# Optimization experiments

Measured on AMD Instinct MI355X. Metric: run time of the kernel, lower is better.

Reference implementation:

```python
import jax, jax.numpy as jnp
import numpy as np

DIM = 512
HEADS = 8
DIM_HEAD = 64
DIM_INNER = HEADS * DIM_HEAD
SCALE = DIM_HEAD ** -0.5


def setup_inputs() -> dict:
    key = jax.random.key(0)
    ks = jax.random.split(key, 8)
    b, n = 2, 1024
    x = jax.random.normal(ks[0], (b, n, DIM), dtype=jnp.float32)
    w = lambda k, i, o: jax.random.normal(k, (i, o), dtype=jnp.float32) * 0.02
    return {
        'x': x,
        'w_q_u': w(ks[1], DIM, DIM_INNER),
        'w_k_u': w(ks[2], DIM, DIM_INNER),
        'w_v_u': w(ks[3], DIM, DIM_INNER),
        'w_q_c': w(ks[4], DIM, DIM_INNER),
        'w_k_c': w(ks[5], DIM, DIM_INNER),
        'w_v_c': w(ks[6], DIM, DIM_INNER),
        'w_out': w(ks[7], DIM_INNER, DIM),
    }


def reference(x, w_q_u, w_k_u, w_v_u, w_q_c, w_k_c, w_v_c, w_out):
    b, n, _ = x.shape

    def proj(w):  # [b,n,dim] -> [b,h,n,d]
        return (x @ w).reshape(b, n, HEADS, DIM_HEAD).transpose(0, 2, 1, 3)

    q_u, k_u, v_u = proj(w_q_u), proj(w_k_u), proj(w_v_u)
    q_c, k_c, v_c = proj(w_q_c), proj(w_k_c), proj(w_v_c)

    idx = jnp.arange(n)
    causal = idx[:, None] >= idx[None, :]  # tril ones (binary causal mask)

    # term1 = (q_c @ v_u^T) * scale, zeroed above diagonal
    term1 = jnp.einsum('bhid,bhjd->bhij', q_c, v_u) * SCALE
    term1 = term1 * causal.astype(term1.dtype)

    # sigmoid term: (q_u @ k_u^T)*scale with lookahead mask tril(-inf, diag=0)
    logits_u = jnp.einsum('bhid,bhjd->bhij', q_u, k_u) * SCALE
    sig = jax.nn.sigmoid(jnp.where(causal, -jnp.inf, logits_u))

    # S_u[i,k] = sum_j term1[i,j] * sig[k,j]
    S_u = jnp.einsum('bhij,bhkj->bhik', term1, sig)

    # S_c: causal-masked QK
    S_c = jnp.einsum('bhid,bhjd->bhij', q_c, k_c) * SCALE
    S_c = jnp.where(causal, S_c, -jnp.inf)

    final_scores = S_c - jax.nn.silu(S_u)
    attn = jax.nn.softmax(final_scores, axis=-1)
    out = jnp.einsum('bhij,bhjd->bhid', attn, v_c)  # [b,h,n,d]
    out = out.transpose(0, 2, 1, 3).reshape(b, n, DIM_INNER)
    return out @ w_out
```

## Files before the change

### kernel.cpp

```cpp
#include <hip/hip_runtime.h>
#include <math.h>


typedef __bf16 bf16x8 __attribute__((ext_vector_type(8)));
typedef float f32x4 __attribute__((ext_vector_type(4)));

#define SCALE 0.125f

#define GLL(g, l) __builtin_amdgcn_global_load_lds(                         \
    (const __attribute__((address_space(1))) void*)(g),                     \
    (__attribute__((address_space(3))) void*)(l), 16, 0, 0)

__device__ __forceinline__ unsigned short f2bf(float f){
  unsigned int x = __builtin_bit_cast(unsigned int, f);
  unsigned int r = (x + 0x7fffu + ((x >> 16) & 1u)) >> 16;
  return (unsigned short)r;
}
__device__ __forceinline__ f32x4 mfma16(bf16x8 a, bf16x8 b, f32x4 c){
  return __builtin_amdgcn_mfma_f32_16x16x32_bf16(a, b, c, 0, 0, 0);
}
__device__ __forceinline__ bf16x8 ld8(const unsigned short* p){
  return *(const bf16x8*)p;
}

__global__ __launch_bounds__(256) void k_prep(
    const float* __restrict__ x,
    const float* __restrict__ w0, const float* __restrict__ w1,
    const float* __restrict__ w2, const float* __restrict__ w3,
    const float* __restrict__ w4, const float* __restrict__ w5,
    const float* __restrict__ w6,
    unsigned short* __restrict__ xb, unsigned short* __restrict__ wT){
  int t = threadIdx.x;
  if (blockIdx.x < 1024){
    int i = blockIdx.x * 256 + t;
    float4 v = ((const float4*)x)[i];
    ushort4 o; o.x = f2bf(v.x); o.y = f2bf(v.y); o.z = f2bf(v.z); o.w = f2bf(v.w);
    ((ushort4*)xb)[i] = o;
    return;
  }
  __shared__ float lds[64 * 65];
  int bx = blockIdx.x - 1024;
  int mat = bx >> 6, tile = bx & 63, tr = tile >> 3, tc = tile & 7;
  int k0 = tr * 64, c0 = tc * 64;
  const float* src;
  switch (mat){
    case 0: src = w0; break; case 1: src = w1; break; case 2: src = w2; break;
    case 3: src = w3; break; case 4: src = w4; break; case 5: src = w5; break;
    default: src = w6; break;
  }
#pragma unroll
  for (int i = 0; i < 4; ++i){
    int r = (t >> 4) + i * 16, c4 = (t & 15) * 4;
    float4 v = *(const float4*)(src + (size_t)(k0 + r) * 512 + c0 + c4);
    lds[r * 65 + c4 + 0] = v.x; lds[r * 65 + c4 + 1] = v.y;
    lds[r * 65 + c4 + 2] = v.z; lds[r * 65 + c4 + 3] = v.w;
  }
  __syncthreads();
  unsigned short* dst = wT + (size_t)mat * 262144;
#pragma unroll
  for (int i = 0; i < 4; ++i){
    int oc = (t >> 4) + i * 16;
    int kq = (t & 15) * 4;
    ushort4 o;
    o.x = f2bf(lds[(kq + 0) * 65 + oc]);
    o.y = f2bf(lds[(kq + 1) * 65 + oc]);
    o.z = f2bf(lds[(kq + 2) * 65 + oc]);
    o.w = f2bf(lds[(kq + 3) * 65 + oc]);
    *(ushort4*)(dst + (size_t)(c0 + oc) * 512 + k0 + kq) = o;
  }
}

__global__ __launch_bounds__(256) void k_proj(
    const unsigned short* __restrict__ xb, const unsigned short* __restrict__ wT,
    unsigned short* __restrict__ P){
  __shared__ unsigned short sA[128 * 32], sB[128 * 32];
  int t = threadIdx.x, lane = t & 63, l16 = lane & 15, quad = lane >> 4;
  int w = t >> 6, wm = w >> 1, wn = w & 1;
  int bx = blockIdx.x;
  int mt = bx / 24, nt = bx - mt * 24;
  int M0 = mt * 128, N0 = nt * 128;
  int matb = N0 >> 9;
  int nin = N0 & 511;
  int srow = (lane >> 2), scol = (lane & 3) * 8;
  const unsigned short* gA = xb + (size_t)(M0 + w*32 + srow) * 512 + scol;
  const unsigned short* gB = wT + (size_t)matb * 262144
                               + (size_t)(nin + w*32 + srow) * 512 + scol;
  unsigned short* lA = sA + (w*32) * 32;
  unsigned short* lB = sB + (w*32) * 32;
  f32x4 acc[4][4] = {};
  for (int k0 = 0; k0 < 512; k0 += 32){
    GLL(gA + k0,            lA);
    GLL(gA + k0 + 16*512,   lA + 16*32);
    GLL(gB + k0,            lB);
    GLL(gB + k0 + 16*512,   lB + 16*32);
    __syncthreads();
    bf16x8 aw[4], ax[4];
#pragma unroll
    for (int fi = 0; fi < 4; ++fi)
      aw[fi] = *(const bf16x8*)(sB + (wn*64 + fi*16 + l16) * 32 + quad * 8);
#pragma unroll
    for (int mi = 0; mi < 4; ++mi)
      ax[mi] = *(const bf16x8*)(sA + (wm*64 + mi*16 + l16) * 32 + quad * 8);
#pragma unroll
    for (int fi = 0; fi < 4; ++fi)
#pragma unroll
      for (int mi = 0; mi < 4; ++mi)
        acc[fi][mi] = mfma16(aw[fi], ax[mi], acc[fi][mi]);
    __syncthreads();
  }
#pragma unroll
  for (int fi = 0; fi < 4; ++fi)
#pragma unroll
    for (int mi = 0; mi < 4; ++mi){
      int row = M0 + wm*64 + mi*16 + l16;
      int b_ = row >> 10, n_ = row & 1023;
      int c0 = N0 + wn*64 + fi*16 + quad*4;
      int h = (c0 & 511) >> 6, d = c0 & 63;
      int bh = b_*8 + h;
      ushort4 o;
      o.x = f2bf(acc[fi][mi][0]); o.y = f2bf(acc[fi][mi][1]);
      o.z = f2bf(acc[fi][mi][2]); o.w = f2bf(acc[fi][mi][3]);
      *(ushort4*)(P + (size_t)(matb*16 + bh) * 65536 + (size_t)n_ * 64 + d) = o;
    }
}

__global__ __launch_bounds__(256) void k_vct(
    const unsigned short* __restrict__ P5, unsigned short* __restrict__ vcT){
  __shared__ unsigned short lds[64 * 72];
  int bh = blockIdx.x >> 4, nt = blockIdx.x & 15;
  int N0 = nt * 64;
  const unsigned short* src = P5 + (size_t)bh * 65536 + (size_t)N0 * 64;
  int t = threadIdx.x;
#pragma unroll
  for (int it = 0; it < 2; ++it){
    int id = it * 256 + t;
    int r = id >> 3, c8 = (id & 7) * 8;
    ushort4 v0 = *(const ushort4*)(src + r * 64 + c8);
    ushort4 v1 = *(const ushort4*)(src + r * 64 + c8 + 4);
    *(ushort4*)(lds + r * 72 + c8) = v0;
    *(ushort4*)(lds + r * 72 + c8 + 4) = v1;
  }
  __syncthreads();
  unsigned short* dst = vcT + (size_t)bh * 65536;
#pragma unroll
  for (int it = 0; it < 2; ++it){
    int id = it * 256 + t;
    int dd = id >> 3, n8 = (id & 7) * 8;
    ushort4 a, b;
    a.x = lds[(n8+0)*72 + dd]; a.y = lds[(n8+1)*72 + dd];
    a.z = lds[(n8+2)*72 + dd]; a.w = lds[(n8+3)*72 + dd];
    b.x = lds[(n8+4)*72 + dd]; b.y = lds[(n8+5)*72 + dd];
    b.z = lds[(n8+6)*72 + dd]; b.w = lds[(n8+7)*72 + dd];
    *(ushort4*)(dst + (size_t)dd * 1024 + N0 + n8) = a;
    *(ushort4*)(dst + (size_t)dd * 1024 + N0 + n8 + 4) = b;
  }
}

__global__ __launch_bounds__(256) void k_qk(
    const unsigned short* __restrict__ P,
    unsigned short* __restrict__ term1, unsigned short* __restrict__ sig){
  int gw = (blockIdx.x * 256 + threadIdx.x) >> 6;
  int lane = threadIdx.x & 63, l16 = lane & 15, quad = lane >> 4;
  int bhm = gw / 576;
  int idx = gw - bhm * 576;
  int bh = bhm >> 1, mat = bhm & 1;
  int B = 0;
  while (idx >= 8 * (B + 1) * (B + 2)) ++B;
  int r2 = idx - 8 * B * (B + 1);
  int per = 2 * (B + 1);
  int mt_in = r2 / per, sub = r2 - mt_in * per;
  int m0 = (B * 8 + mt_in) * 16, n0 = sub * 64;
  if (mat){ m0 = 1008 - m0; n0 = 960 - n0; }
  unsigned short* out = (mat ? sig : term1) + (size_t)bh * 1048576;
  int row = m0 + l16;
  bool zero_tile = mat ? (n0 + 63 <= m0) : (n0 > m0 + 15);
  if (zero_tile){
    ushort4 z = {0, 0, 0, 0};
#pragma unroll
    for (int f = 0; f < 4; ++f)
      *(ushort4*)(out + (size_t)row * 1024 + n0 + f*16 + quad*4) = z;
    return;
  }
  const unsigned short* A  = P + (size_t)((mat ? 0 : 3)*16 + bh) * 65536;
  const unsigned short* Bt = P + (size_t)((mat ? 1 : 2)*16 + bh) * 65536;
  f32x4 acc[4] = {};
  for (int k0 = 0; k0 < 64; k0 += 32){
    bf16x8 bi = ld8(A + (size_t)(m0 + l16) * 64 + k0 + quad * 8);
#pragma unroll
    for (int f = 0; f < 4; ++f){
      bf16x8 aj = ld8(Bt + (size_t)(n0 + f*16 + l16) * 64 + k0 + quad * 8);
      acc[f] = mfma16(aj, bi, acc[f]);
    }
  }
#pragma unroll
  for (int f = 0; f < 4; ++f){
    int c0 = n0 + f*16 + quad*4;
    ushort4 o;
#pragma unroll
    for (int r = 0; r < 4; ++r){
      int col = c0 + r;
      float v = acc[f][r] * SCALE;
      unsigned short res;
      if (mat == 0) res = (col <= row) ? f2bf(v) : (unsigned short)0;
      else          res = (col >  row) ? f2bf(1.f / (1.f + expf(-v))) : (unsigned short)0;
      ((unsigned short*)&o)[r] = res;
    }
    *(ushort4*)(out + (size_t)row * 1024 + c0) = o;
  }
}

__global__ __launch_bounds__(256) void k_scores(
    const unsigned short* __restrict__ P, const unsigned short* __restrict__ term1,
    const unsigned short* __restrict__ sig, float* __restrict__ fin){
  __shared__ unsigned short sA[128 * 32], sB[128 * 32];
  int t = threadIdx.x;
  int bh = blockIdx.x & 15, tt = blockIdx.x >> 4;
  int k = 1, T = 0;
  while (tt >= T + k){ T += k; ++k; }
  int delta = 8 - k;
  int tj = tt - T, ti = tj + delta;
  int M0 = ti * 128, N0 = tj * 128;
  size_t sbase = (size_t)bh * 1048576;
  int lane = t & 63, l16 = lane & 15, quad = lane >> 4;
  int w = t >> 6, wm = w >> 1, wn = w & 1;
  int srow = (lane >> 2), scol = (lane & 3) * 8;
  unsigned short* lA = sA + (w*32) * 32;
  unsigned short* lB = sB + (w*32) * 32;
  f32x4 acc_u[4][4] = {};
  f32x4 acc_c[4][4] = {};
  {
    const unsigned short* gA = term1 + sbase + (size_t)(M0 + w*32 + srow) * 1024 + scol;
    const unsigned short* gB = sig   + sbase + (size_t)(N0 + w*32 + srow) * 1024 + scol;
    int steps = (delta + 1) * 4;
    for (int s = 0; s < steps; ++s){
      int j0 = N0 + s * 32;
      GLL(gA + j0,             lA);
      GLL(gA + j0 + 16*1024,   lA + 16*32);
      GLL(gB + j0,             lB);
      GLL(gB + j0 + 16*1024,   lB + 16*32);
      __syncthreads();
      bf16x8 af[4], bfr[4];
#pragma unroll
      for (int mi = 0; mi < 4; ++mi)
        af[mi] = *(const bf16x8*)(sA + (wm*64 + mi*16 + l16) * 32 + quad * 8);
#pragma unroll
      for (int fi = 0; fi < 4; ++fi)
        bfr[fi] = *(const bf16x8*)(sB + (wn*64 + fi*16 + l16) * 32 + quad * 8);
#pragma unroll
      for (int fi = 0; fi < 4; ++fi)
#pragma unroll
        for (int mi = 0; mi < 4; ++mi)
          acc_u[fi][mi] = mfma16(bfr[fi], af[mi], acc_u[fi][mi]);
      __syncthreads();
    }
  }
  {
    const unsigned short* Qc = P + (size_t)(3*16 + bh) * 65536;
    const unsigned short* Kc = P + (size_t)(4*16 + bh) * 65536;
    const unsigned short* gA = Qc + (size_t)(M0 + w*32 + srow) * 64 + scol;
    const unsigned short* gB = Kc + (size_t)(N0 + w*32 + srow) * 64 + scol;
    for (int s = 0; s < 2; ++s){
      int k0 = s * 32;
      GLL(gA + k0,           lA);
      GLL(gA + k0 + 16*64,   lA + 16*32);
      GLL(gB + k0,           lB);
      GLL(gB + k0 + 16*64,   lB + 16*32);
      __syncthreads();
      bf16x8 af[4], bfr[4];
#pragma unroll
      for (int mi = 0; mi < 4; ++mi)
        af[mi] = *(const bf16x8*)(sA + (wm*64 + mi*16 + l16) * 32 + quad * 8);
#pragma unroll
      for (int fi = 0; fi < 4; ++fi)
        bfr[fi] = *(const bf16x8*)(sB + (wn*64 + fi*16 + l16) * 32 + quad * 8);
#pragma unroll
      for (int fi = 0; fi < 4; ++fi)
#pragma unroll
        for (int mi = 0; mi < 4; ++mi)
          acc_c[fi][mi] = mfma16(bfr[fi], af[mi], acc_c[fi][mi]);
      __syncthreads();
    }
  }
  float* out = fin + sbase;
#pragma unroll
  for (int fi = 0; fi < 4; ++fi)
#pragma unroll
    for (int mi = 0; mi < 4; ++mi){
      int row = M0 + wm*64 + mi*16 + l16;
      int c0 = N0 + wn*64 + fi*16 + quad*4;
      float4 o;
#pragma unroll
      for (int r = 0; r < 4; ++r){
        int col = c0 + r;
        float su = acc_u[fi][mi][r];
        float v = acc_c[fi][mi][r] * SCALE - su / (1.f + expf(-su));
        ((float*)&o)[r] = (col > row) ? -INFINITY : v;
      }
      *(float4*)(out + (size_t)row * 1024 + c0) = o;
    }
}

__global__ __launch_bounds__(256) void k_pv_soft(
    const float* __restrict__ fin, const unsigned short* __restrict__ vcT,
    unsigned short* __restrict__ O){
  __shared__ __align__(16) unsigned char smem[16 * 1032 * 2];
  unsigned short* lp = (unsigned short*)smem;
  float* red = (float*)smem;
  int t = threadIdx.x;
  int bh = blockIdx.x & 15, mt = 63 - (blockIdx.x >> 4);
  int m0 = mt * 16;
  int kceil = ((m0 + 16 + 31) >> 5) << 5;
  {
    int rl = t >> 4, sub = t & 15;
    int rloc = m0 + rl;
    const float* p = fin + (size_t)bh * 1048576 + (size_t)rloc * 1024;
    float4 v[16];
    float m = -INFINITY;
#pragma unroll
    for (int i = 0; i < 16; ++i){
      int c4 = (sub + 16*i) * 4;
      if (c4 < kceil){
        float4 xv = *(const float4*)(p + c4);
        v[i].x = (c4 + 0 <= rloc) ? xv.x : -INFINITY;
        v[i].y = (c4 + 1 <= rloc) ? xv.y : -INFINITY;
        v[i].z = (c4 + 2 <= rloc) ? xv.z : -INFINITY;
        v[i].w = (c4 + 3 <= rloc) ? xv.w : -INFINITY;
        m = fmaxf(m, fmaxf(fmaxf(v[i].x, v[i].y), fmaxf(v[i].z, v[i].w)));
      }
    }
#pragma unroll
    for (int off = 1; off < 16; off <<= 1) m = fmaxf(m, __shfl_xor(m, off));
    float s = 0.f;
#pragma unroll
    for (int i = 0; i < 16; ++i){
      int c4 = (sub + 16*i) * 4;
      if (c4 < kceil){
        v[i].x = expf(v[i].x - m); v[i].y = expf(v[i].y - m);
        v[i].z = expf(v[i].z - m); v[i].w = expf(v[i].w - m);
        s += v[i].x + v[i].y + v[i].z + v[i].w;
      }
    }
#pragma unroll
    for (int off = 1; off < 16; off <<= 1) s += __shfl_xor(s, off);
    float inv = 1.f / s;
#pragma unroll
    for (int i = 0; i < 16; ++i){
      int c4 = (sub + 16*i) * 4;
      if (c4 < kceil){
        ushort4 o;
        o.x = f2bf(v[i].x * inv); o.y = f2bf(v[i].y * inv);
        o.z = f2bf(v[i].z * inv); o.w = f2bf(v[i].w * inv);
        *(ushort4*)(lp + rl * 1032 + c4) = o;
      }
    }
  }
  __syncthreads();
  int lane = t & 63, l16 = lane & 15, quad = lane >> 4, w = t >> 6;
  const unsigned short* Bt = vcT + (size_t)bh * 65536;
  int ktot = kceil >> 5;
  int per = (ktot + 3) >> 2;
  int s0 = w * per, s1 = min(s0 + per, ktot);
  f32x4 acc[4] = {};
  for (int s = s0; s < s1; ++s){
    int k0 = s * 32;
    bf16x8 a = *(const bf16x8*)(lp + l16 * 1032 + k0 + quad * 8);
#pragma unroll
    for (int fi = 0; fi < 4; ++fi){
      bf16x8 b = ld8(Bt + (size_t)(fi*16 + l16) * 1024 + k0 + quad * 8);
      acc[fi] = mfma16(a, b, acc[fi]);
    }
  }
  __syncthreads();
#pragma unroll
  for (int fi = 0; fi < 4; ++fi)
#pragma unroll
    for (int r = 0; r < 4; ++r)
      red[w * 1024 + (quad*4 + r) * 64 + fi*16 + l16] = acc[fi][r];
  __syncthreads();
  float4 a0 = ((const float4*)(red + 0*1024))[t];
  float4 a1 = ((const float4*)(red + 1*1024))[t];
  float4 a2 = ((const float4*)(red + 2*1024))[t];
  float4 a3 = ((const float4*)(red + 3*1024))[t];
  ushort4 o;
  o.x = f2bf(a0.x + a1.x + a2.x + a3.x);
  o.y = f2bf(a0.y + a1.y + a2.y + a3.y);
  o.z = f2bf(a0.z + a1.z + a2.z + a3.z);
  o.w = f2bf(a0.w + a1.w + a2.w + a3.w);
  int e = t * 4, row = e >> 6, col = e & 63;
  *(ushort4*)(O + (size_t)bh * 65536 + (size_t)(m0 + row) * 64 + col) = o;
}

__global__ __launch_bounds__(256) void k_out(
    const unsigned short* __restrict__ O, const unsigned short* __restrict__ woT,
    float* __restrict__ out){
  __shared__ float red[4][1024];
  int t = threadIdx.x, lane = t & 63, l16 = lane & 15, quad = lane >> 4, w = t >> 6;
  int mt = blockIdx.x >> 3, nt = blockIdx.x & 7;
  int m0 = mt * 16, n0 = nt * 64;
  int r_ = m0 + l16, b_ = r_ >> 10, n_ = r_ & 1023;
  f32x4 acc[4] = {};
#pragma unroll
  for (int s = 0; s < 4; ++s){
    int kk = w * 128 + s * 32 + quad * 8;
    int h = kk >> 6, dd = kk & 63;
    bf16x8 a = ld8(O + (size_t)(b_*8 + h) * 65536 + (size_t)n_ * 64 + dd);
#pragma unroll
    for (int fi = 0; fi < 4; ++fi){
      bf16x8 b = ld8(woT + (size_t)(n0 + fi*16 + l16) * 512 + kk);
      acc[fi] = mfma16(a, b, acc[fi]);
    }
  }
#pragma unroll
  for (int fi = 0; fi < 4; ++fi)
#pragma unroll
    for (int r = 0; r < 4; ++r)
      red[w][(quad*4 + r) * 64 + fi*16 + l16] = acc[fi][r];
  __syncthreads();
  float4 a0 = ((const float4*)red[0])[t];
  float4 a1 = ((const float4*)red[1])[t];
  float4 a2 = ((const float4*)red[2])[t];
  float4 a3 = ((const float4*)red[3])[t];
  float4 o;
  o.x = a0.x + a1.x + a2.x + a3.x;
  o.y = a0.y + a1.y + a2.y + a3.y;
  o.z = a0.z + a1.z + a2.z + a3.z;
  o.w = a0.w + a1.w + a2.w + a3.w;
  int e = t * 4, row = e >> 6, col = e & 63;
  *(float4*)(out + (size_t)(m0 + row) * 512 + n0 + col) = o;
}

extern "C" void kernel_launch(void* const* d_in, const int* in_sizes, int n_in,
                              void* d_out, int out_size, void* d_ws, size_t ws_size,
                              hipStream_t stream){
  const float* x = (const float*)d_in[0];
  float* out = (float*)d_out;
  unsigned short* ws = (unsigned short*)d_ws;

  unsigned short* wT    = ws;
  unsigned short* xb    = wT    + (size_t)7  * 262144;
  unsigned short* P     = xb    + (size_t)1048576;
  unsigned short* vcT   = P     + (size_t)96 * 65536;
  unsigned short* term1 = vcT   + (size_t)16 * 65536;
  unsigned short* sig   = term1 + (size_t)16 * 1048576;
  unsigned short* O     = sig   + (size_t)16 * 1048576;
  float*          fin   = (float*)(O + (size_t)16 * 65536);

  k_prep<<<1472, 256, 0, stream>>>(
      x,
      (const float*)d_in[1], (const float*)d_in[2], (const float*)d_in[3],
      (const float*)d_in[4], (const float*)d_in[5], (const float*)d_in[6],
      (const float*)d_in[7], xb, wT);
  k_proj<<<384, 256, 0, stream>>>(xb, wT, P);
  k_vct<<<256, 256, 0, stream>>>(P + (size_t)5*16*65536, vcT);
  k_qk<<<4608, 256, 0, stream>>>(P, term1, sig);
  k_scores<<<576, 256, 0, stream>>>(P, term1, sig, fin);
  k_pv_soft<<<1024, 256, 0, stream>>>(fin, vcT, O);
  k_out<<<1024, 256, 0, stream>>>(O, wT + (size_t)6 * 262144, out);
}
```

Measured before the change: 180.6 us.

## Store final scores in bf16, merge V transpose into QK launch, drop LDS staging

The fp32 final-scores buffer between k_scores and the softmax/PV kernel becomes bf16. This halves the write and read traffic of a 16x1024x1024 intermediate, and the causal mask now lives only in the consumer. The separate V-transpose kernel is folded into the QK kernel as extra blocks, which removes one launch. The Q_c·K_c phase of k_scores now loads its MFMA operands directly from global memory instead of staging them in LDS, which drops two barriers per step. The risk is bf16 precision loss on the logits before softmax, plus possibly less coalesced direct loads.

```diff
diff --git a/kernel.cpp b/kernel.cpp
--- a/kernel.cpp
+++ b/kernel.cpp
@@ -15,6 +15,10 @@
   unsigned int x = __builtin_bit_cast(unsigned int, f);
   unsigned int r = (x + 0x7fffu + ((x >> 16) & 1u)) >> 16;
   return (unsigned short)r;
+}
+__device__ __forceinline__ float bf2f(unsigned short u){
+  unsigned int x = ((unsigned int)u) << 16;
+  return __builtin_bit_cast(float, x);
 }
 __device__ __forceinline__ f32x4 mfma16(bf16x8 a, bf16x8 b, f32x4 c){
   return __builtin_amdgcn_mfma_f32_16x16x32_bf16(a, b, c, 0, 0, 0);
@@ -124,43 +128,43 @@
     }
 }
 
-__global__ __launch_bounds__(256) void k_vct(
-    const unsigned short* __restrict__ P5, unsigned short* __restrict__ vcT){
+__global__ __launch_bounds__(256) void k_qk_vct(
+    const unsigned short* __restrict__ P,
+    unsigned short* __restrict__ term1, unsigned short* __restrict__ sig,
+    unsigned short* __restrict__ vcT){
   __shared__ unsigned short lds[64 * 72];
-  int bh = blockIdx.x >> 4, nt = blockIdx.x & 15;
-  int N0 = nt * 64;
-  const unsigned short* src = P5 + (size_t)bh * 65536 + (size_t)N0 * 64;
   int t = threadIdx.x;
-#pragma unroll
-  for (int it = 0; it < 2; ++it){
-    int id = it * 256 + t;
-    int r = id >> 3, c8 = (id & 7) * 8;
-    ushort4 v0 = *(const ushort4*)(src + r * 64 + c8);
-    ushort4 v1 = *(const ushort4*)(src + r * 64 + c8 + 4);
-    *(ushort4*)(lds + r * 72 + c8) = v0;
-    *(ushort4*)(lds + r * 72 + c8 + 4) = v1;
-  }
-  __syncthreads();
-  unsigned short* dst = vcT + (size_t)bh * 65536;
-#pragma unroll
-  for (int it = 0; it < 2; ++it){
-    int id = it * 256 + t;
-    int dd = id >> 3, n8 = (id & 7) * 8;
-    ushort4 a, b;
-    a.x = lds[(n8+0)*72 + dd]; a.y = lds[(n8+1)*72 + dd];
-    a.z = lds[(n8+2)*72 + dd]; a.w = lds[(n8+3)*72 + dd];
-    b.x = lds[(n8+4)*72 + dd]; b.y = lds[(n8+5)*72 + dd];
-    b.z = lds[(n8+6)*72 + dd]; b.w = lds[(n8+7)*72 + dd];
-    *(ushort4*)(dst + (size_t)dd * 1024 + N0 + n8) = a;
-    *(ushort4*)(dst + (size_t)dd * 1024 + N0 + n8 + 4) = b;
-  }
-}
-
-__global__ __launch_bounds__(256) void k_qk(
-    const unsigned short* __restrict__ P,
-    unsigned short* __restrict__ term1, unsigned short* __restrict__ sig){
-  int gw = (blockIdx.x * 256 + threadIdx.x) >> 6;
-  int lane = threadIdx.x & 63, l16 = lane & 15, quad = lane >> 4;
+  if (blockIdx.x < 256){
+    int bh = blockIdx.x >> 4, nt = blockIdx.x & 15;
+    int N0 = nt * 64;
+    const unsigned short* src = P + (size_t)(5*16 + bh) * 65536 + (size_t)N0 * 64;
+#pragma unroll
+    for (int it = 0; it < 2; ++it){
+      int id = it * 256 + t;
+      int r = id >> 3, c8 = (id & 7) * 8;
+      ushort4 v0 = *(const ushort4*)(src + r * 64 + c8);
+      ushort4 v1 = *(const ushort4*)(src + r * 64 + c8 + 4);
+      *(ushort4*)(lds + r * 72 + c8) = v0;
+      *(ushort4*)(lds + r * 72 + c8 + 4) = v1;
+    }
+    __syncthreads();
+    unsigned short* dst = vcT + (size_t)bh * 65536;
+#pragma unroll
+    for (int it = 0; it < 2; ++it){
+      int id = it * 256 + t;
+      int dd = id >> 3, n8 = (id & 7) * 8;
+      ushort4 a, b;
+      a.x = lds[(n8+0)*72 + dd]; a.y = lds[(n8+1)*72 + dd];
+      a.z = lds[(n8+2)*72 + dd]; a.w = lds[(n8+3)*72 + dd];
+      b.x = lds[(n8+4)*72 + dd]; b.y = lds[(n8+5)*72 + dd];
+      b.z = lds[(n8+6)*72 + dd]; b.w = lds[(n8+7)*72 + dd];
+      *(ushort4*)(dst + (size_t)dd * 1024 + N0 + n8) = a;
+      *(ushort4*)(dst + (size_t)dd * 1024 + N0 + n8 + 4) = b;
+    }
+    return;
+  }
+  int gw = ((blockIdx.x - 256) * 256 + t) >> 6;
+  int lane = t & 63, l16 = lane & 15, quad = lane >> 4;
   int bhm = gw / 576;
   int idx = gw - bhm * 576;
   int bh = bhm >> 1, mat = bhm & 1;
@@ -211,7 +215,7 @@
 
 __global__ __launch_bounds__(256) void k_scores(
     const unsigned short* __restrict__ P, const unsigned short* __restrict__ term1,
-    const unsigned short* __restrict__ sig, float* __restrict__ fin){
+    const unsigned short* __restrict__ sig, unsigned short* __restrict__ finb){
   __shared__ unsigned short sA[128 * 32], sB[128 * 32];
   int t = threadIdx.x;
   int bh = blockIdx.x & 15, tt = blockIdx.x >> 4;
@@ -257,51 +261,42 @@
   {
     const unsigned short* Qc = P + (size_t)(3*16 + bh) * 65536;
     const unsigned short* Kc = P + (size_t)(4*16 + bh) * 65536;
-    const unsigned short* gA = Qc + (size_t)(M0 + w*32 + srow) * 64 + scol;
-    const unsigned short* gB = Kc + (size_t)(N0 + w*32 + srow) * 64 + scol;
-    for (int s = 0; s < 2; ++s){
-      int k0 = s * 32;
-      GLL(gA + k0,           lA);
-      GLL(gA + k0 + 16*64,   lA + 16*32);
-      GLL(gB + k0,           lB);
-      GLL(gB + k0 + 16*64,   lB + 16*32);
-      __syncthreads();
+#pragma unroll
+    for (int k0 = 0; k0 < 64; k0 += 32){
       bf16x8 af[4], bfr[4];
 #pragma unroll
       for (int mi = 0; mi < 4; ++mi)
-        af[mi] = *(const bf16x8*)(sA + (wm*64 + mi*16 + l16) * 32 + quad * 8);
+        af[mi] = ld8(Qc + (size_t)(M0 + wm*64 + mi*16 + l16) * 64 + k0 + quad * 8);
 #pragma unroll
       for (int fi = 0; fi < 4; ++fi)
-        bfr[fi] = *(const bf16x8*)(sB + (wn*64 + fi*16 + l16) * 32 + quad * 8);
+        bfr[fi] = ld8(Kc + (size_t)(N0 + wn*64 + fi*16 + l16) * 64 + k0 + quad * 8);
 #pragma unroll
       for (int fi = 0; fi < 4; ++fi)
 #pragma unroll
         for (int mi = 0; mi < 4; ++mi)
           acc_c[fi][mi] = mfma16(bfr[fi], af[mi], acc_c[fi][mi]);
-      __syncthreads();
-    }
-  }
-  float* out = fin + sbase;
+    }
+  }
+  unsigned short* out = finb + sbase;
 #pragma unroll
   for (int fi = 0; fi < 4; ++fi)
 #pragma unroll
     for (int mi = 0; mi < 4; ++mi){
       int row = M0 + wm*64 + mi*16 + l16;
       int c0 = N0 + wn*64 + fi*16 + quad*4;
-      float4 o;
+      ushort4 o;
 #pragma unroll
       for (int r = 0; r < 4; ++r){
-        int col = c0 + r;
         float su = acc_u[fi][mi][r];
         float v = acc_c[fi][mi][r] * SCALE - su / (1.f + expf(-su));
-        ((float*)&o)[r] = (col > row) ? -INFINITY : v;
+        ((unsigned short*)&o)[r] = f2bf(v);
       }
-      *(float4*)(out + (size_t)row * 1024 + c0) = o;
+      *(ushort4*)(out + (size_t)row * 1024 + c0) = o;
     }
 }
 
 __global__ __launch_bounds__(256) void k_pv_soft(
-    const float* __restrict__ fin, const unsigned short* __restrict__ vcT,
+    const unsigned short* __restrict__ finb, const unsigned short* __restrict__ vcT,
     unsigned short* __restrict__ O){
   __shared__ __align__(16) unsigned char smem[16 * 1032 * 2];
   unsigned short* lp = (unsigned short*)smem;
@@ -313,44 +308,52 @@
   {
     int rl = t >> 4, sub = t & 15;
     int rloc = m0 + rl;
-    const float* p = fin + (size_t)bh * 1048576 + (size_t)rloc * 1024;
-    float4 v[16];
+    const unsigned short* p = finb + (size_t)bh * 1048576 + (size_t)rloc * 1024;
+    float v[8][8];
     float m = -INFINITY;
 #pragma unroll
-    for (int i = 0; i < 16; ++i){
-      int c4 = (sub + 16*i) * 4;
-      if (c4 < kceil){
-        float4 xv = *(const float4*)(p + c4);
-        v[i].x = (c4 + 0 <= rloc) ? xv.x : -INFINITY;
-        v[i].y = (c4 + 1 <= rloc) ? xv.y : -INFINITY;
-        v[i].z = (c4 + 2 <= rloc) ? xv.z : -INFINITY;
-        v[i].w = (c4 + 3 <= rloc) ? xv.w : -INFINITY;
-        m = fmaxf(m, fmaxf(fmaxf(v[i].x, v[i].y), fmaxf(v[i].z, v[i].w)));
+    for (int i = 0; i < 8; ++i){
+      int c8 = (sub + 16*i) * 8;
+      if (c8 < kceil){
+        ushort4 u0 = *(const ushort4*)(p + c8);
+        ushort4 u1 = *(const ushort4*)(p + c8 + 4);
+        float vv[8] = {bf2f(u0.x), bf2f(u0.y), bf2f(u0.z), bf2f(u0.w),
+                       bf2f(u1.x), bf2f(u1.y), bf2f(u1.z), bf2f(u1.w)};
+#pragma unroll
+        for (int e = 0; e < 8; ++e){
+          v[i][e] = (c8 + e <= rloc) ? vv[e] : -INFINITY;
+          m = fmaxf(m, v[i][e]);
+        }
       }
     }
 #pragma unroll
     for (int off = 1; off < 16; off <<= 1) m = fmaxf(m, __shfl_xor(m, off));
     float s = 0.f;
 #pragma unroll
-    for (int i = 0; i < 16; ++i){
-      int c4 = (sub + 16*i) * 4;
-      if (c4 < kceil){
-        v[i].x = expf(v[i].x - m); v[i].y = expf(v[i].y - m);
-        v[i].z = expf(v[i].z - m); v[i].w = expf(v[i].w - m);
-        s += v[i].x + v[i].y + v[i].z + v[i].w;
+    for (int i = 0; i < 8; ++i){
+      int c8 = (sub + 16*i) * 8;
+      if (c8 < kceil){
+#pragma unroll
+        for (int e = 0; e < 8; ++e){
+          v[i][e] = expf(v[i][e] - m);
+          s += v[i][e];
+        }
       }
     }
 #pragma unroll
     for (int off = 1; off < 16; off <<= 1) s += __shfl_xor(s, off);
     float inv = 1.f / s;
 #pragma unroll
-    for (int i = 0; i < 16; ++i){
-      int c4 = (sub + 16*i) * 4;
-      if (c4 < kceil){
-        ushort4 o;
-        o.x = f2bf(v[i].x * inv); o.y = f2bf(v[i].y * inv);
-        o.z = f2bf(v[i].z * inv); o.w = f2bf(v[i].w * inv);
-        *(ushort4*)(lp + rl * 1032 + c4) = o;
+    for (int i = 0; i < 8; ++i){
+      int c8 = (sub + 16*i) * 8;
+      if (c8 < kceil){
+        ushort4 o0, o1;
+        o0.x = f2bf(v[i][0] * inv); o0.y = f2bf(v[i][1] * inv);
+        o0.z = f2bf(v[i][2] * inv); o0.w = f2bf(v[i][3] * inv);
+        o1.x = f2bf(v[i][4] * inv); o1.y = f2bf(v[i][5] * inv);
+        o1.z = f2bf(v[i][6] * inv); o1.w = f2bf(v[i][7] * inv);
+        *(ushort4*)(lp + rl * 1032 + c8) = o0;
+        *(ushort4*)(lp + rl * 1032 + c8 + 4) = o1;
       }
     }
   }
@@ -443,7 +446,7 @@
   unsigned short* term1 = vcT   + (size_t)16 * 65536;
   unsigned short* sig   = term1 + (size_t)16 * 1048576;
   unsigned short* O     = sig   + (size_t)16 * 1048576;
-  float*          fin   = (float*)(O + (size_t)16 * 65536);
+  unsigned short* finb  = O     + (size_t)16 * 65536;
 
   k_prep<<<1472, 256, 0, stream>>>(
       x,
@@ -451,9 +454,8 @@
       (const float*)d_in[4], (const float*)d_in[5], (const float*)d_in[6],
       (const float*)d_in[7], xb, wT);
   k_proj<<<384, 256, 0, stream>>>(xb, wT, P);
-  k_vct<<<256, 256, 0, stream>>>(P + (size_t)5*16*65536, vcT);
-  k_qk<<<4608, 256, 0, stream>>>(P, term1, sig);
-  k_scores<<<576, 256, 0, stream>>>(P, term1, sig, fin);
-  k_pv_soft<<<1024, 256, 0, stream>>>(fin, vcT, O);
+  k_qk_vct<<<4864, 256, 0, stream>>>(P, term1, sig, vcT);
+  k_scores<<<576, 256, 0, stream>>>(P, term1, sig, finb);
+  k_pv_soft<<<1024, 256, 0, stream>>>(finb, vcT, O);
   k_out<<<1024, 256, 0, stream>>>(O, wT + (size_t)6 * 262144, out);
 }
```

Result: faster. 176.7 us (-2.2%).
